# Performance work log

Measured on AMD Instinct MI355X. Metric: run time of the kernel, lower is better.

The kernel has to match this reference:

```python
import jax, jax.numpy as jnp
import numpy as np

EPS_LN = 1e-6
EPS_NORM = 1e-12
MAX_SCALE_MUL = float(np.log(100.0))
H = 16  # num_heads


def _ln(x):
    # affine-free LayerNorm over last dim (torch uses biased variance)
    mu = jnp.mean(x, axis=-1, keepdims=True)
    var = jnp.mean((x - mu) ** 2, axis=-1, keepdims=True)
    return (x - mu) / jnp.sqrt(var + EPS_LN)


def _l2norm(x):
    n = jnp.sqrt(jnp.sum(x * x, axis=-1, keepdims=True))
    return x / jnp.maximum(n, EPS_NORM)


def setup_inputs() -> dict:
    key = jax.random.key(0)
    ks = jax.random.split(key, 12)
    B, L, C = 4, 1024, 1024
    Ccond, Dff = 1024, 4096
    s = lambda fan: 1.0 / np.sqrt(fan)
    return {
        "x": jax.random.normal(ks[0], (B, L, C), jnp.float32),
        "cond": jax.random.normal(ks[1], (B, Ccond), jnp.float32),
        "mat_qkv_w": jax.random.normal(ks[2], (3 * C, C), jnp.float32) * s(C),
        "q_bias": jnp.zeros((C,), jnp.float32),
        "v_bias": jnp.zeros((C,), jnp.float32),
        "scale_mul": jnp.full((1, H, 1, 1), np.log(4.0), jnp.float32),
        "proj_w": jax.random.normal(ks[3], (C, C), jnp.float32) * s(C),
        "proj_b": jnp.zeros((C,), jnp.float32),
        "ada_w": jax.random.normal(ks[4], (6 * C, Ccond), jnp.float32) * s(Ccond),
        "ada_b": jnp.zeros((6 * C,), jnp.float32),
        "fc1_w": jax.random.normal(ks[5], (Dff, C), jnp.float32) * s(C),
        "fc1_b": jnp.zeros((Dff,), jnp.float32),
        "fc2_w": jax.random.normal(ks[6], (C, Dff), jnp.float32) * s(Dff),
        "fc2_b": jnp.zeros((C,), jnp.float32),
    }


def reference(x, cond, mat_qkv_w, q_bias, v_bias, scale_mul, proj_w, proj_b,
              ada_w, ada_b, fc1_w, fc1_b, fc2_w, fc2_b):
    B, L, C = x.shape
    hd = C // H

    # AdaLN modulation params: SiLU -> Linear -> [B,1,6,C]
    ada = jax.nn.silu(cond) @ ada_w.T + ada_b
    ada = ada.reshape(B, 1, 6, C)
    gamma1, gamma2, scale1, scale2, shift1, shift2 = [ada[:, :, i] for i in range(6)]

    # --- attention branch ---
    x1 = _ln(x) * (scale1 + 1.0) + shift1
    qkv_bias = jnp.concatenate([q_bias, jnp.zeros_like(q_bias), v_bias])
    qkv = (x1 @ mat_qkv_w.T + qkv_bias).reshape(B, L, 3, H, hd)
    q, k, v = [jnp.transpose(qkv[:, :, i], (0, 2, 1, 3)) for i in range(3)]  # [B,H,L,hd]

    sm = jnp.exp(jnp.minimum(scale_mul, MAX_SCALE_MUL))  # [1,H,1,1]
    q = _l2norm(q) * sm
    k = _l2norm(k)

    scores = jnp.einsum('bhqd,bhkd->bhqk', q, k)  # scale = 1.0 under l2 norm
    probs = jax.nn.softmax(scores, axis=-1)
    o = jnp.einsum('bhqk,bhkd->bhqd', probs, v)
    o = jnp.transpose(o, (0, 2, 1, 3)).reshape(B, L, C)
    attn_out = o @ proj_w.T + proj_b
    x = x + attn_out * gamma1

    # --- FFN branch ---
    x2 = _ln(x) * (scale2 + 1.0) + shift2
    h = jax.nn.gelu(x2 @ fc1_w.T + fc1_b, approximate=False)
    ffn_out = h @ fc2_w.T + fc2_b
    x = x + ffn_out * gamma2
    return x
```

## Files before the change

### kernel.cpp

```cpp
#include <hip/hip_runtime.h>

typedef __bf16 bf16x8_t __attribute__((ext_vector_type(8)));
typedef bf16x8_t bf16x8 __attribute__((may_alias));
typedef float f32x4 __attribute__((ext_vector_type(4)));
typedef unsigned short u16x4 __attribute__((ext_vector_type(4)));
typedef unsigned short u16x8 __attribute__((ext_vector_type(8)));

#define DEV __device__ __forceinline__

DEV float b2f(unsigned short u) {
  union { unsigned int i; float f; } x; x.i = ((unsigned int)u) << 16; return x.f;
}
DEV unsigned short f2b(float f) {
  union { float f; unsigned int i; } x; x.f = f;
  return (unsigned short)((x.i + 0x7fffu + ((x.i >> 16) & 1u)) >> 16);
}

#define AS1(p) ((__attribute__((address_space(1))) void*)(p))
#define AS3(p) ((__attribute__((address_space(3))) void*)(p))

__global__ __launch_bounds__(256) void k_ada(const float* __restrict__ cond,
                                             const float* __restrict__ w,
                                             const float* __restrict__ bias,
                                             float* __restrict__ out) {
  __shared__ float sc[4096];
  int tt = threadIdx.x;
#pragma unroll
  for (int i = 0; i < 16; ++i) {
    float v = cond[tt + i * 256];
    sc[tt + i * 256] = v / (1.f + __expf(-v));
  }
  __syncthreads();
  int j = blockIdx.x * 4 + (tt >> 6);
  int lane = tt & 63;
  const float* wr = w + (size_t)j * 1024;
  float s0 = 0.f, s1 = 0.f, s2 = 0.f, s3 = 0.f;
#pragma unroll
  for (int u = 0; u < 4; ++u) {
    int k = u * 256 + lane * 4;
    float4 a = *(const float4*)(wr + k);
    float4 c0 = *(const float4*)(sc + k);
    float4 c1 = *(const float4*)(sc + 1024 + k);
    float4 c2 = *(const float4*)(sc + 2048 + k);
    float4 c3 = *(const float4*)(sc + 3072 + k);
    s0 += a.x * c0.x + a.y * c0.y + a.z * c0.z + a.w * c0.w;
    s1 += a.x * c1.x + a.y * c1.y + a.z * c1.z + a.w * c1.w;
    s2 += a.x * c2.x + a.y * c2.y + a.z * c2.z + a.w * c2.w;
    s3 += a.x * c3.x + a.y * c3.y + a.z * c3.z + a.w * c3.w;
  }
#pragma unroll
  for (int o = 1; o < 64; o <<= 1) {
    s0 += __shfl_xor(s0, o); s1 += __shfl_xor(s1, o);
    s2 += __shfl_xor(s2, o); s3 += __shfl_xor(s3, o);
  }
  if (lane == 0) {
    float bb = bias[j];
    out[j] = s0 + bb;
    out[6144 + j] = s1 + bb;
    out[12288 + j] = s2 + bb;
    out[18432 + j] = s3 + bb;
  }
}

__global__ __launch_bounds__(256) void k_castall(const float* __restrict__ q,
                                                 const float* __restrict__ p,
                                                 const float* __restrict__ f1,
                                                 const float* __restrict__ f2,
                                                 unsigned short* __restrict__ wq,
                                                 unsigned short* __restrict__ wp,
                                                 unsigned short* __restrict__ wf1,
                                                 unsigned short* __restrict__ wf2) {
  int i = blockIdx.x * 256 + threadIdx.x;
  for (int v = i; v < 3145728; v += 524288) {
    const float* s; unsigned short* d; int off;
    if (v < 786432) { s = q; d = wq; off = v; }
    else if (v < 1048576) { s = p; d = wp; off = v - 786432; }
    else if (v < 2097152) { s = f1; d = wf1; off = v - 1048576; }
    else { s = f2; d = wf2; off = v - 2097152; }
    float4 x = ((const float4*)s)[off];
    u16x4 o;
    o[0] = f2b(x.x); o[1] = f2b(x.y); o[2] = f2b(x.z); o[3] = f2b(x.w);
    *(u16x4*)(d + (size_t)off * 4) = o;
  }
}

__global__ __launch_bounds__(256) void k_ln_mod(const float* __restrict__ src,
                                                const float* __restrict__ ada,
                                                unsigned short* __restrict__ dst,
                                                int sidx, int hidx) {
  int row = blockIdx.x;
  int b = row >> 10;
  int t = threadIdx.x, lane = t & 63, wv = t >> 6;
  float4 v = *(const float4*)(src + (size_t)row * 1024 + t * 4);
  float s = v.x + v.y + v.z + v.w;
  float s2 = v.x * v.x + v.y * v.y + v.z * v.z + v.w * v.w;
#pragma unroll
  for (int o = 1; o < 64; o <<= 1) { s += __shfl_xor(s, o); s2 += __shfl_xor(s2, o); }
  __shared__ float red[8];
  if (lane == 0) { red[wv] = s; red[4 + wv] = s2; }
  __syncthreads();
  float ts = red[0] + red[1] + red[2] + red[3];
  float ts2 = red[4] + red[5] + red[6] + red[7];
  float mu = ts * (1.f / 1024.f);
  float var = ts2 * (1.f / 1024.f) - mu * mu;
  float rstd = rsqrtf(var + 1e-6f);
  const float* ar = ada + (size_t)b * 6144;
  float4 sc = *(const float4*)(ar + sidx * 1024 + t * 4);
  float4 sh = *(const float4*)(ar + hidx * 1024 + t * 4);
  u16x4 o;
  o[0] = f2b((v.x - mu) * rstd * (sc.x + 1.f) + sh.x);
  o[1] = f2b((v.y - mu) * rstd * (sc.y + 1.f) + sh.y);
  o[2] = f2b((v.z - mu) * rstd * (sc.z + 1.f) + sh.z);
  o[3] = f2b((v.w - mu) * rstd * (sc.w + 1.f) + sh.w);
  *(u16x4*)(dst + (size_t)row * 1024 + t * 4) = o;
}

template <int EPI, int SPLIT>
__global__ __launch_bounds__(512, 1) void k_gemm256(const unsigned short* __restrict__ A,
                                                    const unsigned short* __restrict__ W,
                                                    int N, int lda, int ldb, int nt,
                                                    const float* __restrict__ bias,
                                                    const float* __restrict__ qb,
                                                    const float* __restrict__ vb,
                                                    unsigned short* __restrict__ o0,
                                                    unsigned short* __restrict__ o1,
                                                    unsigned short* __restrict__ o2,
                                                    unsigned short* __restrict__ o3) {
  __shared__ unsigned short LDS[65536];
  const int tid = threadIdx.x;
  const int wv = tid >> 6, lane = tid & 63;
  const int fr = lane & 15, fg = lane >> 4;
  const int wm = wv >> 2, wn = wv & 3;

  const int cpx = gridDim.x >> 3;
  int wid = ((int)blockIdx.x & 7) * cpx + ((int)blockIdx.x >> 3);
  int sp = 0;
  if (SPLIT > 1) { sp = wid & (SPLIT - 1); wid >>= 2; }
  const int nx = N >> 8;
  const int m0 = (wid / nx) * 256, n0 = (wid % nx) * 256;
  const int kbase = sp * (nt << 6);
  unsigned short* outp = (SPLIT > 1) ? (sp == 0 ? o0 : sp == 1 ? o1 : sp == 2 ? o2 : o3) : o0;

  const int sRow = lane >> 2;
  const int sCh = (lane & 3) ^ ((lane >> 3) & 3);
  const unsigned short* aG = A + (size_t)(m0 + wv * 16 + sRow) * lda + kbase + sCh * 8;
  const unsigned short* bG = W + (size_t)(n0 + wv * 16 + sRow) * ldb + kbase + sCh * 8;

#define STQ4(qi_)                                                                              \
  {                                                                                            \
    const int wr_ = ((qi_)&3) * 16384;                                                         \
    const int ko_ = (qi_)*32;                                                                  \
    __builtin_amdgcn_global_load_lds(AS1(aG + ko_), AS3(LDS + wr_ + wv * 512), 16, 0, 0);      \
    __builtin_amdgcn_global_load_lds(AS1(aG + (size_t)128 * lda + ko_),                        \
                                     AS3(LDS + wr_ + 4096 + wv * 512), 16, 0, 0);              \
    __builtin_amdgcn_global_load_lds(AS1(bG + ko_), AS3(LDS + wr_ + 8192 + wv * 512), 16, 0, 0);\
    __builtin_amdgcn_global_load_lds(AS1(bG + (size_t)128 * ldb + ko_),                        \
                                     AS3(LDS + wr_ + 12288 + wv * 512), 16, 0, 0);             \
  }

  const int rswz = (fr >> 1) & 3;
  const int aOff = (wm * 128 + fr) * 32 + ((fg ^ rswz) << 3);
  const int bOff = 8192 + (wn * 64 + fr) * 32 + ((fg ^ rswz) << 3);

  f32x4 zz = {0.f, 0.f, 0.f, 0.f};
  f32x4 acc[8][4];
#pragma unroll
  for (int i = 0; i < 8; ++i)
#pragma unroll
    for (int j = 0; j < 4; ++j) acc[i][j] = zz;

#pragma unroll
  for (int q = 0; q < 3; ++q) STQ4(q);
  asm volatile("s_waitcnt vmcnt(8)" ::: "memory");
  __builtin_amdgcn_s_barrier();

#define LDSV(off) (*(const bf16x8*)(LDS + (off)))

  const int ns = 2 * nt;
  for (int st = 0; st < ns; ++st) {
    if (st + 3 < ns) STQ4(st + 3);
    const int rb = (st & 3) * 16384;
    bf16x8 bf0 = LDSV(rb + bOff);
    bf16x8 bf1 = LDSV(rb + bOff + 512);
    bf16x8 bf2 = LDSV(rb + bOff + 1024);
    bf16x8 bf3 = LDSV(rb + bOff + 1536);
    bf16x8 af[8];
#pragma unroll
    for (int mi = 0; mi < 8; ++mi) af[mi] = LDSV(rb + aOff + mi * 512);
#pragma unroll
    for (int mi = 0; mi < 8; ++mi) {
      acc[mi][0] = __builtin_amdgcn_mfma_f32_16x16x32_bf16(af[mi], bf0, acc[mi][0], 0, 0, 0);
      acc[mi][1] = __builtin_amdgcn_mfma_f32_16x16x32_bf16(af[mi], bf1, acc[mi][1], 0, 0, 0);
      acc[mi][2] = __builtin_amdgcn_mfma_f32_16x16x32_bf16(af[mi], bf2, acc[mi][2], 0, 0, 0);
      acc[mi][3] = __builtin_amdgcn_mfma_f32_16x16x32_bf16(af[mi], bf3, acc[mi][3], 0, 0, 0);
    }
    if (st < ns - 3) {
      asm volatile("s_waitcnt vmcnt(8)" ::: "memory");
    } else if (st == ns - 3) {
      asm volatile("s_waitcnt vmcnt(4)" ::: "memory");
    } else if (st == ns - 2) {
      asm volatile("s_waitcnt vmcnt(0)" ::: "memory");
    }
    __builtin_amdgcn_s_barrier();
  }

#pragma unroll
  for (int mi = 0; mi < 8; ++mi) {
#pragma unroll
    for (int ni = 0; ni < 4; ++ni) {
#pragma unroll
      for (int r = 0; r < 4; ++r) {
        int m = m0 + wm * 128 + mi * 16 + fg * 4 + r;
        int n = n0 + wn * 64 + ni * 16 + fr;
        float v = acc[mi][ni][r];
        if constexpr (EPI == 0) {
          float bb = (n < 1024) ? qb[n] : ((n < 2048) ? 0.f : vb[n - 2048]);
          outp[(size_t)m * N + n] = f2b(v + bb);
        } else if constexpr (EPI == 2) {
          float z = v + bias[n];
          float u = z * (0.7978845608f + 0.0356774081f * z * z);
          float e = __expf(2.f * u);
          float th = 1.f - 2.f / (e + 1.f);
          outp[(size_t)m * N + n] = f2b(0.5f * z * (1.f + th));
        } else {
          outp[(size_t)m * N + n] = f2b(v);
        }
      }
    }
  }
#undef STQ4
#undef LDSV
}

__global__ __launch_bounds__(256) void k_fc2red(const unsigned short* __restrict__ P0,
                                                const unsigned short* __restrict__ P1,
                                                const unsigned short* __restrict__ P2,
                                                const unsigned short* __restrict__ P3,
                                                const float* __restrict__ xmid,
                                                const float* __restrict__ bias,
                                                const float* __restrict__ ada,
                                                float* __restrict__ out) {
  size_t idx = ((size_t)blockIdx.x * 256 + threadIdx.x) * 8;
  int n = (int)(idx & 1023);
  int b = (int)(idx >> 20);
  u16x8 v0 = *(const u16x8*)(P0 + idx);
  u16x8 v1 = *(const u16x8*)(P1 + idx);
  u16x8 v2 = *(const u16x8*)(P2 + idx);
  u16x8 v3 = *(const u16x8*)(P3 + idx);
  const float* gp = ada + (size_t)b * 6144 + 1024 + n;
  const float* bp = bias + n;
  const float* xp = xmid + idx;
  float* op = out + idx;
#pragma unroll
  for (int i = 0; i < 8; ++i) {
    float sum = b2f(v0[i]) + b2f(v1[i]) + b2f(v2[i]) + b2f(v3[i]);
    op[i] = xp[i] + (sum + bp[i]) * gp[i];
  }
}

__global__ __launch_bounds__(512) void k_gemm8(const unsigned short* __restrict__ A,
                                               const unsigned short* __restrict__ W,
                                               int M, int N, int K, int Khalf,
                                               const float* __restrict__ bias,
                                               const float* __restrict__ resid,
                                               const float* __restrict__ ada,
                                               float* __restrict__ outp) {
  __shared__ unsigned short SM[49152];
  const int t = threadIdx.x, lane = t & 63, wv = t >> 6;
  const int grp = wv >> 2, w4 = wv & 3;
  const int wr = w4 >> 1, wc = w4 & 1;
  const int cpx = gridDim.x >> 3;
  const int orig = blockIdx.x;
  const int wid = (orig & 7) * cpx + (orig >> 3);
  const int nx = N >> 7;
  const int m0 = (wid / nx) * 128, n0 = (wid % nx) * 128;

  f32x4 zz = {0.f, 0.f, 0.f, 0.f};
  f32x4 acc[4][4];
#pragma unroll
  for (int i = 0; i < 4; ++i)
#pragma unroll
    for (int j = 0; j < 4; ++j) acc[i][j] = zz;

  const int srow = lane >> 2, scol = (lane & 3) * 8;
  const int kbase = grp * Khalf;
  const unsigned short* aSrc0 = A + (size_t)(m0 + w4 * 16 + srow) * K + kbase + scol;
  const unsigned short* aSrc1 = aSrc0 + (size_t)64 * K;
  const unsigned short* bSrc0 = W + (size_t)(n0 + w4 * 16 + srow) * K + kbase + scol;
  const unsigned short* bSrc1 = bSrc0 + (size_t)64 * K;
  unsigned short* grpA = SM + grp * 24576;

  const int fr = lane & 15, fk = (lane >> 4) * 8;

#define STG8(buf_, k0_)                                                                            \
  {                                                                                                \
    __builtin_amdgcn_global_load_lds(AS1(aSrc0 + (k0_)), AS3(grpA + (buf_)*8192 + w4 * 512), 16, 0, 0); \
    __builtin_amdgcn_global_load_lds(AS1(aSrc1 + (k0_)), AS3(grpA + (buf_)*8192 + 2048 + w4 * 512), 16, 0, 0); \
    __builtin_amdgcn_global_load_lds(AS1(bSrc0 + (k0_)), AS3(grpA + (buf_)*8192 + 4096 + w4 * 512), 16, 0, 0); \
    __builtin_amdgcn_global_load_lds(AS1(bSrc1 + (k0_)), AS3(grpA + (buf_)*8192 + 6144 + w4 * 512), 16, 0, 0); \
  }

  const int nsteps = Khalf >> 5;
  STG8(0, 0);
  STG8(1, 32);
  asm volatile("s_waitcnt vmcnt(4)" ::: "memory");
  __builtin_amdgcn_s_barrier();

  for (int i = 0; i < nsteps; ++i) {
    const int buf = i % 3;
    if (i + 2 < nsteps) STG8((i + 2) % 3, (i + 2) * 32);
    const unsigned short* aRd = grpA + buf * 8192 + (wr * 64 + fr) * 32 + fk;
    const unsigned short* bRd = grpA + buf * 8192 + 4096 + (wc * 64 + fr) * 32 + fk;
    bf16x8 af[4], bfv[4];
#pragma unroll
    for (int q = 0; q < 4; ++q) af[q] = *(const bf16x8*)(aRd + q * 512);
#pragma unroll
    for (int q = 0; q < 4; ++q) bfv[q] = *(const bf16x8*)(bRd + q * 512);
#pragma unroll
    for (int mi = 0; mi < 4; ++mi)
#pragma unroll
      for (int ni = 0; ni < 4; ++ni)
        acc[mi][ni] = __builtin_amdgcn_mfma_f32_16x16x32_bf16(af[mi], bfv[ni], acc[mi][ni], 0, 0, 0);
    if (i < nsteps - 1) {
      if (i + 2 < nsteps) {
        asm volatile("s_waitcnt vmcnt(4)" ::: "memory");
      } else {
        asm volatile("s_waitcnt vmcnt(0)" ::: "memory");
      }
      __builtin_amdgcn_s_barrier();
    }
  }
  __syncthreads();

  float* xch = (float*)SM;
#pragma unroll
  for (int c = 0; c < 16; ++c) {
    if (grp == 1)
      *(f32x4*)&xch[c * 1024 + (w4 * 64 + lane) * 4] = acc[c >> 2][c & 3];
  }
  __syncthreads();
  if (grp == 1) return;
#pragma unroll
  for (int c = 0; c < 16; ++c) {
    f32x4 p = *(const f32x4*)&xch[c * 1024 + (w4 * 64 + lane) * 4];
    acc[c >> 2][c & 3] += p;
  }

  const int fg = lane >> 4;
#pragma unroll
  for (int mi = 0; mi < 4; ++mi) {
#pragma unroll
    for (int ni = 0; ni < 4; ++ni) {
#pragma unroll
      for (int r = 0; r < 4; ++r) {
        int m = m0 + wr * 64 + mi * 16 + fg * 4 + r;
        int n = n0 + wc * 64 + ni * 16 + fr;
        float v = acc[mi][ni][r];
        float g = ada[(size_t)(m >> 10) * 6144 + n];
        outp[(size_t)m * N + n] = resid[(size_t)m * N + n] + (v + bias[n]) * g;
      }
    }
  }
#undef STG8
}

__global__ __launch_bounds__(256) void k_qknorm(const unsigned short* __restrict__ qkv,
                                                const float* __restrict__ smul,
                                                unsigned short* __restrict__ Qn,
                                                unsigned short* __restrict__ Kn) {
  int row = blockIdx.x;
  int b = row >> 10, l = row & 1023;
  int t = threadIdx.x;
  int h = t >> 4, sl = t & 15;
  const unsigned short* base = qkv + (size_t)row * 3072 + h * 64 + sl * 4;
  size_t off = ((size_t)(b * 16 + h) * 1024 + l) * 64 + sl * 4;
  {
    u16x4 qv = *(const u16x4*)base;
    float q0 = b2f(qv[0]), q1 = b2f(qv[1]), q2 = b2f(qv[2]), q3 = b2f(qv[3]);
    float ss = q0 * q0 + q1 * q1 + q2 * q2 + q3 * q3;
#pragma unroll
    for (int o = 1; o < 16; o <<= 1) ss += __shfl_xor(ss, o);
    float sm = __expf(fminf(smul[h], 4.6051701859880914f));
    float qs = sm / fmaxf(sqrtf(ss), 1e-12f);
    u16x4 o; o[0] = f2b(q0 * qs); o[1] = f2b(q1 * qs); o[2] = f2b(q2 * qs); o[3] = f2b(q3 * qs);
    *(u16x4*)(Qn + off) = o;
  }
  {
    u16x4 kv = *(const u16x4*)(base + 1024);
    float k0 = b2f(kv[0]), k1 = b2f(kv[1]), k2 = b2f(kv[2]), k3 = b2f(kv[3]);
    float ss = k0 * k0 + k1 * k1 + k2 * k2 + k3 * k3;
#pragma unroll
    for (int o = 1; o < 16; o <<= 1) ss += __shfl_xor(ss, o);
    float ks = 1.f / fmaxf(sqrtf(ss), 1e-12f);
    u16x4 o; o[0] = f2b(k0 * ks); o[1] = f2b(k1 * ks); o[2] = f2b(k2 * ks); o[3] = f2b(k3 * ks);
    *(u16x4*)(Kn + off) = o;
  }
}

__global__ __launch_bounds__(256) void k_vtrans(const unsigned short* __restrict__ qkv,
                                                unsigned short* __restrict__ Vt) {
  int bh = blockIdx.y, b = bh >> 4, h = bh & 15;
  int l0 = blockIdx.x * 64;
  __shared__ unsigned short tile[64][72];
  int t = threadIdx.x;
  int lr = t >> 2, dp = (t & 3) * 16;
  const unsigned short* src = qkv + (size_t)(b * 1024 + l0 + lr) * 3072 + 2048 + h * 64 + dp;
  *(u16x8*)&tile[lr][dp] = *(const u16x8*)src;
  *(u16x8*)&tile[lr][dp + 8] = *(const u16x8*)(src + 8);
  __syncthreads();
  int d = t >> 2, lp = (t & 3) * 16;
  unsigned short ov[16];
#pragma unroll
  for (int j = 0; j < 16; ++j) {
    int p = lp + j;
    int l = ((p >> 5) * 2 + ((p >> 2) & 1)) * 16 + ((p >> 3) & 3) * 4 + (p & 3);
    ov[j] = tile[l][d];
  }
  unsigned short* dst = Vt + ((size_t)bh * 64 + d) * 1024 + l0 + lp;
  *(u16x8*)dst = *(u16x8*)&ov[0];
  *(u16x8*)(dst + 8) = *(u16x8*)&ov[8];
}

__global__ __launch_bounds__(256) void k_attn(const unsigned short* __restrict__ Qn,
                                              const unsigned short* __restrict__ Kn,
                                              const unsigned short* __restrict__ Vt,
                                              const float* __restrict__ smul,
                                              unsigned short* __restrict__ O) {
  const int qt = blockIdx.x, bh = blockIdx.y;
  const int b = bh >> 4, h = bh & 15;
  const int t = threadIdx.x, lane = t & 63, wv = t >> 6;
  const int fr = lane & 15, fg = lane >> 4;
  __shared__ unsigned short Kb[2][4096];
  __shared__ unsigned short Vb[2][4096];

  const int q0 = qt * 128 + wv * 32;
  const unsigned short* qp = Qn + ((size_t)bh * 1024 + q0 + fr) * 64 + fg * 8;
  bf16x8 qf00 = *(const bf16x8*)qp;
  bf16x8 qf01 = *(const bf16x8*)(qp + 32);
  bf16x8 qf10 = *(const bf16x8*)(qp + 1024);
  bf16x8 qf11 = *(const bf16x8*)(qp + 1024 + 32);

  const float M = __expf(fminf(smul[h], 4.6051701859880914f));

  const int srow = lane >> 3, sc = lane & 7;
  const int xr = (sc ^ srow) * 8;
  const unsigned short* kp0 = Kn + (size_t)bh * 65536 + (size_t)(wv * 16 + srow) * 64 + xr;
  const unsigned short* kp1 = kp0 + 8 * 64;
  const unsigned short* vp0 = Vt + (size_t)bh * 65536 + (size_t)(wv * 16 + srow) * 1024 + xr;
  const unsigned short* vp1 = vp0 + 8 * 1024;

  f32x4 zz = {0.f, 0.f, 0.f, 0.f};
  f32x4 oa0[4], oa1[4];
#pragma unroll
  for (int i = 0; i < 4; ++i) { oa0[i] = zz; oa1[i] = zz; }
  float ls0 = 0.f, ls1 = 0.f;

  {
    unsigned short* kd = &Kb[0][wv * 1024];
    unsigned short* vd = &Vb[0][wv * 1024];
    __builtin_amdgcn_global_load_lds(AS1(kp0), AS3(kd), 16, 0, 0);
    __builtin_amdgcn_global_load_lds(AS1(kp1), AS3(kd + 512), 16, 0, 0);
    __builtin_amdgcn_global_load_lds(AS1(vp0), AS3(vd), 16, 0, 0);
    __builtin_amdgcn_global_load_lds(AS1(vp1), AS3(vd + 512), 16, 0, 0);
  }
  __syncthreads();

  int cur = 0;
  for (int kv = 0; kv < 1024; kv += 64) {
    const int nxt = cur ^ 1;
    if (kv + 64 < 1024) {
      const int ko = (kv + 64) * 64;
      const int vo = kv + 64;
      unsigned short* kd = &Kb[nxt][wv * 1024];
      unsigned short* vd = &Vb[nxt][wv * 1024];
      __builtin_amdgcn_global_load_lds(AS1(kp0 + ko), AS3(kd), 16, 0, 0);
      __builtin_amdgcn_global_load_lds(AS1(kp1 + ko), AS3(kd + 512), 16, 0, 0);
      __builtin_amdgcn_global_load_lds(AS1(vp0 + vo), AS3(vd), 16, 0, 0);
      __builtin_amdgcn_global_load_lds(AS1(vp1 + vo), AS3(vd + 512), 16, 0, 0);
    }

    f32x4 s0[4], s1[4];
#pragma unroll
    for (int ct = 0; ct < 4; ++ct) {
      const int row = ct * 16 + fr, r7 = row & 7;
      const unsigned short* kr = &Kb[cur][row * 64];
      bf16x8 kf0 = *(const bf16x8*)(kr + ((fg ^ r7) << 3));
      bf16x8 kf1 = *(const bf16x8*)(kr + (((4 + fg) ^ r7) << 3));
      f32x4 z0 = __builtin_amdgcn_mfma_f32_16x16x32_bf16(kf0, qf00, zz, 0, 0, 0);
      s0[ct] = __builtin_amdgcn_mfma_f32_16x16x32_bf16(kf1, qf01, z0, 0, 0, 0);
      f32x4 z1 = __builtin_amdgcn_mfma_f32_16x16x32_bf16(kf0, qf10, zz, 0, 0, 0);
      s1[ct] = __builtin_amdgcn_mfma_f32_16x16x32_bf16(kf1, qf11, z1, 0, 0, 0);
    }

    bf16x8 pa0[2], pa1[2];
#pragma unroll
    for (int kg = 0; kg < 2; ++kg) {
      bf16x8 a0, a1;
#pragma unroll
      for (int c2 = 0; c2 < 2; ++c2) {
#pragma unroll
        for (int r = 0; r < 4; ++r) {
          float e0 = __expf(s0[kg * 2 + c2][r] - M);
          float e1 = __expf(s1[kg * 2 + c2][r] - M);
          ls0 += e0; ls1 += e1;
          a0[c2 * 4 + r] = (__bf16)e0;
          a1[c2 * 4 + r] = (__bf16)e1;
        }
      }
      pa0[kg] = a0; pa1[kg] = a1;
    }

#pragma unroll
    for (int kg = 0; kg < 2; ++kg) {
#pragma unroll
      for (int dt = 0; dt < 4; ++dt) {
        const int row = dt * 16 + fr, r7 = row & 7;
        bf16x8 vf = *(const bf16x8*)(&Vb[cur][row * 64] + ((((kg << 2) + fg) ^ r7) << 3));
        oa0[dt] = __builtin_amdgcn_mfma_f32_16x16x32_bf16(pa0[kg], vf, oa0[dt], 0, 0, 0);
        oa1[dt] = __builtin_amdgcn_mfma_f32_16x16x32_bf16(pa1[kg], vf, oa1[dt], 0, 0, 0);
      }
    }
    __syncthreads();
    cur = nxt;
  }

  ls0 += __shfl_xor(ls0, 16); ls0 += __shfl_xor(ls0, 32);
  ls1 += __shfl_xor(ls1, 16); ls1 += __shfl_xor(ls1, 32);

#pragma unroll
  for (int r = 0; r < 4; ++r) {
    float i0 = 1.f / __shfl(ls0, fg * 4 + r);
    float i1 = 1.f / __shfl(ls1, fg * 4 + r);
    unsigned short* ob = O + ((size_t)(b * 1024 + q0 + fg * 4 + r)) * 1024 + h * 64 + fr;
#pragma unroll
    for (int dt = 0; dt < 4; ++dt) {
      ob[dt * 16] = f2b(oa0[dt][r] * i0);
      ob[(size_t)16 * 1024 + dt * 16] = f2b(oa1[dt][r] * i1);
    }
  }
}

extern "C" void kernel_launch(void* const* d_in, const int* in_sizes, int n_in,
                              void* d_out, int out_size, void* d_ws, size_t ws_size,
                              hipStream_t stream) {
  const float* x        = (const float*)d_in[0];
  const float* cond     = (const float*)d_in[1];
  const float* qkv_w    = (const float*)d_in[2];
  const float* q_bias   = (const float*)d_in[3];
  const float* v_bias   = (const float*)d_in[4];
  const float* scale_mul= (const float*)d_in[5];
  const float* proj_w   = (const float*)d_in[6];
  const float* proj_b   = (const float*)d_in[7];
  const float* ada_w    = (const float*)d_in[8];
  const float* ada_b    = (const float*)d_in[9];
  const float* fc1_w    = (const float*)d_in[10];
  const float* fc1_b    = (const float*)d_in[11];
  const float* fc2_w    = (const float*)d_in[12];
  const float* fc2_b    = (const float*)d_in[13];
  float* out = (float*)d_out;
  char* ws = (char*)d_ws;

  unsigned short* WQ   = (unsigned short*)(ws + 0);
  unsigned short* WP   = (unsigned short*)(ws + 6291456);
  unsigned short* WF1  = (unsigned short*)(ws + 8388608);
  unsigned short* WF2  = (unsigned short*)(ws + 16777216);
  float*          ADA  = (float*)(ws + 25182208);
  unsigned short* X1   = (unsigned short*)(ws + 25280512);
  unsigned short* QKVB = (unsigned short*)(ws + 33669120);
  unsigned short* QN   = (unsigned short*)(ws + 58834944);
  unsigned short* KN   = (unsigned short*)(ws + 67223552);
  unsigned short* VT   = (unsigned short*)(ws + 75612160);
  unsigned short* OB   = (unsigned short*)(ws + 84000768);
  float*          XMID = (float*)(ws + 33669120);
  unsigned short* HB   = (unsigned short*)(ws + 50446336);
  unsigned short* FP0  = (unsigned short*)(ws + 0);
  unsigned short* FP1  = (unsigned short*)(ws + 8388608);
  unsigned short* FP2  = (unsigned short*)(ws + 25280512);
  unsigned short* FP3  = (unsigned short*)(ws + 84000768);

  (void)in_sizes; (void)n_in; (void)out_size; (void)ws_size;

  k_ada<<<1536, 256, 0, stream>>>(cond, ada_w, ada_b, ADA);
  k_castall<<<2048, 256, 0, stream>>>(qkv_w, proj_w, fc1_w, fc2_w, WQ, WP, WF1, WF2);

  k_ln_mod<<<4096, 256, 0, stream>>>(x, ADA, X1, 2, 4);
  k_gemm256<0, 1><<<192, 512, 0, stream>>>(X1, WQ, 3072, 1024, 1024, 16,
                                           nullptr, q_bias, v_bias, QKVB, nullptr, nullptr, nullptr);
  k_qknorm<<<4096, 256, 0, stream>>>(QKVB, scale_mul, QN, KN);
  k_vtrans<<<dim3(16, 64), 256, 0, stream>>>(QKVB, VT);
  k_attn<<<dim3(8, 64), 256, 0, stream>>>(QN, KN, VT, scale_mul, OB);
  k_gemm8<<<256, 512, 0, stream>>>(OB, WP, 4096, 1024, 1024, 512,
                                   proj_b, x, ADA, XMID);
  k_ln_mod<<<4096, 256, 0, stream>>>(XMID, ADA, X1, 3, 5);
  k_gemm256<2, 1><<<256, 512, 0, stream>>>(X1, WF1, 4096, 1024, 1024, 16,
                                           fc1_b, nullptr, nullptr, HB, nullptr, nullptr, nullptr);
  k_gemm256<4, 4><<<256, 512, 0, stream>>>(HB, WF2, 1024, 4096, 4096, 16,
                                           nullptr, nullptr, nullptr, FP0, FP1, FP2, FP3);
  k_fc2red<<<2048, 256, 0, stream>>>(FP0, FP1, FP2, FP3, XMID, fc2_b, ADA, out);
}
```

Measured before the change: 227.6 us.

## Restructure GEMM main loop into fine-grained interleaved load/MFMA phases

Replaces the 4-stage per-k-step pipeline in the bf16 GEMM with a double-buffered 64-wide K tile, split into eight phases per iteration. Each phase issues one slice of global->LDS loads, reads a half of the A fragments, and runs 16 MFMAs under raised wave priority, with explicit barriers and waitcnts. The LDS swizzle is also removed. The aim is to hide memory latency better by interleaving issue with compute. In exchange it adds more barriers per step and may bring back LDS bank conflicts without the XOR swizzle.

```diff
diff --git a/kernel.cpp b/kernel.cpp
--- a/kernel.cpp
+++ b/kernel.cpp
@@ -141,78 +141,109 @@
   const int kbase = sp * (nt << 6);
   unsigned short* outp = (SPLIT > 1) ? (sp == 0 ? o0 : sp == 1 ? o1 : sp == 2 ? o2 : o3) : o0;
 
-  const int sRow = lane >> 2;
-  const int sCh = (lane & 3) ^ ((lane >> 3) & 3);
-  const unsigned short* aG = A + (size_t)(m0 + wv * 16 + sRow) * lda + kbase + sCh * 8;
-  const unsigned short* bG = W + (size_t)(n0 + wv * 16 + sRow) * ldb + kbase + sCh * 8;
-
-#define STQ4(qi_)                                                                              \
-  {                                                                                            \
-    const int wr_ = ((qi_)&3) * 16384;                                                         \
-    const int ko_ = (qi_)*32;                                                                  \
-    __builtin_amdgcn_global_load_lds(AS1(aG + ko_), AS3(LDS + wr_ + wv * 512), 16, 0, 0);      \
-    __builtin_amdgcn_global_load_lds(AS1(aG + (size_t)128 * lda + ko_),                        \
-                                     AS3(LDS + wr_ + 4096 + wv * 512), 16, 0, 0);              \
-    __builtin_amdgcn_global_load_lds(AS1(bG + ko_), AS3(LDS + wr_ + 8192 + wv * 512), 16, 0, 0);\
-    __builtin_amdgcn_global_load_lds(AS1(bG + (size_t)128 * ldb + ko_),                        \
-                                     AS3(LDS + wr_ + 12288 + wv * 512), 16, 0, 0);             \
-  }
-
-  const int rswz = (fr >> 1) & 3;
-  const int aOff = (wm * 128 + fr) * 32 + ((fg ^ rswz) << 3);
-  const int bOff = 8192 + (wn * 64 + fr) * 32 + ((fg ^ rswz) << 3);
+  const unsigned short* aG = A + (size_t)(m0 + (tid >> 2)) * lda + kbase + (tid & 3) * 8;
+  const unsigned short* bG = W + (size_t)(n0 + (tid >> 2)) * ldb + kbase + (tid & 3) * 8;
+
+#define STG(t_, op_, ks_)                                                                    \
+  {                                                                                          \
+    const unsigned short* g_ = ((op_) ? bG : aG) + (t_) * 64 + (ks_) * 32;                   \
+    const int ld_ = (op_) ? ldb : lda;                                                       \
+    unsigned short* d_ = LDS + ((t_) & 1) * 32768 + (op_) * 16384 + (ks_) * 8192 + wv * 512; \
+    __builtin_amdgcn_global_load_lds(AS1(g_), AS3(d_), 16, 0, 0);                            \
+    __builtin_amdgcn_global_load_lds(AS1(g_ + (size_t)128 * ld_), AS3(d_ + 4096), 16, 0, 0); \
+  }
 
   f32x4 zz = {0.f, 0.f, 0.f, 0.f};
   f32x4 acc[8][4];
 #pragma unroll
   for (int i = 0; i < 8; ++i)
 #pragma unroll
-    for (int j = 0; j < 4; ++j) acc[i][j] = zz;
-
-#pragma unroll
-  for (int q = 0; q < 3; ++q) STQ4(q);
-  asm volatile("s_waitcnt vmcnt(8)" ::: "memory");
+    for (int jj = 0; jj < 4; ++jj) acc[i][jj] = zz;
+
+  STG(0, 0, 0); STG(0, 1, 0); STG(0, 0, 1); STG(0, 1, 1);
+  STG(1, 0, 0); STG(1, 1, 0);
+  asm volatile("s_waitcnt vmcnt(4)" ::: "memory");
   __builtin_amdgcn_s_barrier();
 
-#define LDSV(off) (*(const bf16x8*)(LDS + (off)))
-
-  const int ns = 2 * nt;
-  for (int st = 0; st < ns; ++st) {
-    if (st + 3 < ns) STQ4(st + 3);
-    const int rb = (st & 3) * 16384;
-    bf16x8 bf0 = LDSV(rb + bOff);
-    bf16x8 bf1 = LDSV(rb + bOff + 512);
-    bf16x8 bf2 = LDSV(rb + bOff + 1024);
-    bf16x8 bf3 = LDSV(rb + bOff + 1536);
-    bf16x8 af[8];
-#pragma unroll
-    for (int mi = 0; mi < 8; ++mi) af[mi] = LDSV(rb + aOff + mi * 512);
-#pragma unroll
-    for (int mi = 0; mi < 8; ++mi) {
-      acc[mi][0] = __builtin_amdgcn_mfma_f32_16x16x32_bf16(af[mi], bf0, acc[mi][0], 0, 0, 0);
-      acc[mi][1] = __builtin_amdgcn_mfma_f32_16x16x32_bf16(af[mi], bf1, acc[mi][1], 0, 0, 0);
-      acc[mi][2] = __builtin_amdgcn_mfma_f32_16x16x32_bf16(af[mi], bf2, acc[mi][2], 0, 0, 0);
-      acc[mi][3] = __builtin_amdgcn_mfma_f32_16x16x32_bf16(af[mi], bf3, acc[mi][3], 0, 0, 0);
-    }
-    if (st < ns - 3) {
-      asm volatile("s_waitcnt vmcnt(8)" ::: "memory");
-    } else if (st == ns - 3) {
-      asm volatile("s_waitcnt vmcnt(4)" ::: "memory");
-    } else if (st == ns - 2) {
-      asm volatile("s_waitcnt vmcnt(0)" ::: "memory");
-    }
-    __builtin_amdgcn_s_barrier();
+  bf16x8 bq0, bq1, bq2, bq3;
+
+#define MFMA16(mh_)                                                                             \
+  acc[(mh_)*4+0][0] = __builtin_amdgcn_mfma_f32_16x16x32_bf16(a0_, bq0, acc[(mh_)*4+0][0],0,0,0); \
+  acc[(mh_)*4+1][0] = __builtin_amdgcn_mfma_f32_16x16x32_bf16(a1_, bq0, acc[(mh_)*4+1][0],0,0,0); \
+  acc[(mh_)*4+2][0] = __builtin_amdgcn_mfma_f32_16x16x32_bf16(a2_, bq0, acc[(mh_)*4+2][0],0,0,0); \
+  acc[(mh_)*4+3][0] = __builtin_amdgcn_mfma_f32_16x16x32_bf16(a3_, bq0, acc[(mh_)*4+3][0],0,0,0); \
+  acc[(mh_)*4+0][1] = __builtin_amdgcn_mfma_f32_16x16x32_bf16(a0_, bq1, acc[(mh_)*4+0][1],0,0,0); \
+  acc[(mh_)*4+1][1] = __builtin_amdgcn_mfma_f32_16x16x32_bf16(a1_, bq1, acc[(mh_)*4+1][1],0,0,0); \
+  acc[(mh_)*4+2][1] = __builtin_amdgcn_mfma_f32_16x16x32_bf16(a2_, bq1, acc[(mh_)*4+2][1],0,0,0); \
+  acc[(mh_)*4+3][1] = __builtin_amdgcn_mfma_f32_16x16x32_bf16(a3_, bq1, acc[(mh_)*4+3][1],0,0,0); \
+  acc[(mh_)*4+0][2] = __builtin_amdgcn_mfma_f32_16x16x32_bf16(a0_, bq2, acc[(mh_)*4+0][2],0,0,0); \
+  acc[(mh_)*4+1][2] = __builtin_amdgcn_mfma_f32_16x16x32_bf16(a1_, bq2, acc[(mh_)*4+1][2],0,0,0); \
+  acc[(mh_)*4+2][2] = __builtin_amdgcn_mfma_f32_16x16x32_bf16(a2_, bq2, acc[(mh_)*4+2][2],0,0,0); \
+  acc[(mh_)*4+3][2] = __builtin_amdgcn_mfma_f32_16x16x32_bf16(a3_, bq2, acc[(mh_)*4+3][2],0,0,0); \
+  acc[(mh_)*4+0][3] = __builtin_amdgcn_mfma_f32_16x16x32_bf16(a0_, bq3, acc[(mh_)*4+0][3],0,0,0); \
+  acc[(mh_)*4+1][3] = __builtin_amdgcn_mfma_f32_16x16x32_bf16(a1_, bq3, acc[(mh_)*4+1][3],0,0,0); \
+  acc[(mh_)*4+2][3] = __builtin_amdgcn_mfma_f32_16x16x32_bf16(a2_, bq3, acc[(mh_)*4+2][3],0,0,0); \
+  acc[(mh_)*4+3][3] = __builtin_amdgcn_mfma_f32_16x16x32_bf16(a3_, bq3, acc[(mh_)*4+3][3],0,0,0);
+
+#define PH(bufo_, ks_, mh_, stT_, stOp_, stKs_, VM_)                                     \
+  {                                                                                      \
+    const int rb_ = (bufo_) + (ks_) * 8192;                                              \
+    if ((mh_) == 0) {                                                                    \
+      const int bo_ = rb_ + 16384 + (wn * 64 + fr) * 32 + (fg << 3);                     \
+      bq0 = *(const bf16x8*)(LDS + bo_);                                                 \
+      bq1 = *(const bf16x8*)(LDS + bo_ + 512);                                           \
+      bq2 = *(const bf16x8*)(LDS + bo_ + 1024);                                          \
+      bq3 = *(const bf16x8*)(LDS + bo_ + 1536);                                          \
+    }                                                                                    \
+    const int ao_ = rb_ + (wm * 128 + (mh_) * 64 + fr) * 32 + (fg << 3);                 \
+    bf16x8 a0_ = *(const bf16x8*)(LDS + ao_);                                            \
+    bf16x8 a1_ = *(const bf16x8*)(LDS + ao_ + 512);                                      \
+    bf16x8 a2_ = *(const bf16x8*)(LDS + ao_ + 1024);                                     \
+    bf16x8 a3_ = *(const bf16x8*)(LDS + ao_ + 1536);                                     \
+    if ((stT_) < nt) { STG(stT_, stOp_, stKs_); }                                        \
+    __builtin_amdgcn_s_barrier();                                                        \
+    asm volatile("s_waitcnt lgkmcnt(0)" ::: "memory");                                   \
+    __builtin_amdgcn_sched_barrier(0);                                                   \
+    __builtin_amdgcn_s_setprio(1);                                                       \
+    MFMA16(mh_)                                                                          \
+    __builtin_amdgcn_s_setprio(0);                                                       \
+    asm volatile("s_waitcnt vmcnt(" VM_ ")" ::: "memory");                               \
+    __builtin_amdgcn_s_barrier();                                                        \
+  }
+
+  const int ni = nt >> 1;
+  for (int j = 0; j < ni - 1; ++j) {
+    const int t1 = 2 * j + 1, t2 = 2 * j + 2, t3 = 2 * j + 3;
+    PH(0,     0, 0, t1, 0, 1, "8")
+    PH(0,     0, 1, t1, 1, 1, "8")
+    PH(0,     1, 0, t2, 0, 0, "8")
+    PH(0,     1, 1, t2, 1, 0, "8")
+    PH(32768, 0, 0, t2, 0, 1, "8")
+    PH(32768, 0, 1, t2, 1, 1, "8")
+    PH(32768, 1, 0, t3, 0, 0, "8")
+    PH(32768, 1, 1, t3, 1, 0, "8")
+  }
+  {
+    const int t1 = nt - 1;
+    PH(0,     0, 0, t1, 0, 1, "8")
+    PH(0,     0, 1, t1, 1, 1, "8")
+    PH(0,     1, 0, nt, 0, 0, "8")
+    PH(0,     1, 1, nt, 1, 0, "4")
+    PH(32768, 0, 0, nt, 0, 1, "8")
+    PH(32768, 0, 1, nt, 1, 1, "0")
+    PH(32768, 1, 0, nt, 0, 0, "8")
+    PH(32768, 1, 1, nt, 1, 0, "0")
   }
 
 #pragma unroll
   for (int mi = 0; mi < 8; ++mi) {
 #pragma unroll
-    for (int ni = 0; ni < 4; ++ni) {
+    for (int nni = 0; nni < 4; ++nni) {
 #pragma unroll
       for (int r = 0; r < 4; ++r) {
         int m = m0 + wm * 128 + mi * 16 + fg * 4 + r;
-        int n = n0 + wn * 64 + ni * 16 + fr;
-        float v = acc[mi][ni][r];
+        int n = n0 + wn * 64 + nni * 16 + fr;
+        float v = acc[mi][nni][r];
         if constexpr (EPI == 0) {
           float bb = (n < 1024) ? qb[n] : ((n < 2048) ? 0.f : vb[n - 2048]);
           outp[(size_t)m * N + n] = f2b(v + bb);
@@ -228,8 +259,9 @@
       }
     }
   }
-#undef STQ4
-#undef LDSV
+#undef STG
+#undef MFMA16
+#undef PH
 }
 
 __global__ __launch_bounds__(256) void k_fc2red(const unsigned short* __restrict__ P0,
```

Measured after the change: 232.8 us. +2.3%, slower.
